# Kernel tuning notes

Hardware: AMD Instinct MI355X
Metric: run time of the kernel (lower is better)

## Reference

```python
import jax, jax.numpy as jnp
import numpy as np

HIDDEN = 1024


def setup_inputs() -> dict:
    key = jax.random.key(0)
    ks = jax.random.split(key, 8)
    B, S, H = 64, 2048, HIDDEN
    scale = 1.0 / np.sqrt(H)
    return {
        "decoder_hidden": jax.random.normal(ks[0], (B, H), jnp.float32),
        "encoder_outputs": jax.random.normal(ks[1], (B, S, 2 * H), jnp.float32),
        "coverage": jax.random.uniform(ks[2], (B, S), jnp.float32),
        "mask": jnp.ones((B, S), jnp.int32),
        # parameters (nn.Linear weight layout: (out, in); we store transposed for x @ W)
        "W_h": jax.random.normal(ks[3], (2 * H, H), jnp.float32) * scale,
        "W_d": jax.random.normal(ks[4], (H, H), jnp.float32) * scale,
        "W_c": jax.random.normal(ks[5], (1, H), jnp.float32) * scale,
        "v": jax.random.normal(ks[6], (H, 1), jnp.float32) * scale,
    }


def reference(decoder_hidden, encoder_outputs, coverage, mask, W_h, W_d, W_c, v):
    # energy: (B, S, H) = tanh(enc@W_h + dec@W_d broadcast over S + coverage*W_c)
    enc_proj = jnp.einsum("bse,eh->bsh", encoder_outputs, W_h)
    dec_proj = (decoder_hidden @ W_d)[:, None, :]            # (B,1,H)
    cov_proj = coverage[:, :, None] * W_c[0][None, None, :]  # (B,S,H)
    energy = jnp.tanh(enc_proj + dec_proj + cov_proj)
    scores = jnp.einsum("bsh,h->bs", energy, v[:, 0])        # (B,S)
    scores = jnp.where(mask == 0, jnp.float32(-10000.0), scores)
    attn_weights = jax.nn.softmax(scores, axis=1)            # (B,S)
    coverage_new = coverage + attn_weights
    context = jnp.einsum("bs,bse->be", attn_weights, encoder_outputs)  # (B,2H)
    return (context, attn_weights, coverage_new)
```

## Files before the change

### kernel.cpp

```cpp
#include <hip/hip_runtime.h>
#include <hip/hip_bf16.h>
#include <stdint.h>

#define BATCH 64
#define SEQ   2048
#define HID   1024
#define EDIM  2048

#define BM 64
#define BN 512
#define BK 32
#define KSTEPS (EDIM / BK)
#define BS (BATCH * SEQ)
#define SMEM_BYTES 76032

typedef __bf16 bf16x8 __attribute__((ext_vector_type(8)));
typedef float  f32x4a __attribute__((ext_vector_type(4)));

__device__ __forceinline__ unsigned short f2bf(float x) {
    __hip_bfloat16 h = __float2bfloat16(x);
    return __builtin_bit_cast(unsigned short, h);
}

__device__ __forceinline__ uint4 pack8(f32x4a f0, f32x4a f1) {
    uint4 r;
    r.x = (unsigned)f2bf(f0.x) | ((unsigned)f2bf(f0.y) << 16);
    r.y = (unsigned)f2bf(f0.z) | ((unsigned)f2bf(f0.w) << 16);
    r.z = (unsigned)f2bf(f1.x) | ((unsigned)f2bf(f1.y) << 16);
    r.w = (unsigned)f2bf(f1.z) | ((unsigned)f2bf(f1.w) << 16);
    return r;
}

__device__ __forceinline__ void gload16(const void* g, void* l) {
    __builtin_amdgcn_global_load_lds(
        (const __attribute__((address_space(1))) void*)g,
        (__attribute__((address_space(3))) void*)l, 16, 0, 0);
}

__device__ __forceinline__ f32x4a ntload4(const float* p) {
    return __builtin_nontemporal_load((const f32x4a*)p);
}

__device__ __forceinline__ int a_addr(int row, int g) {
    int slot = g ^ ((row & 3) ^ ((row >> 2) & 3));
    return (row << 6) + (slot << 4);
}

__global__ void wh_transpose_kernel(const float* __restrict__ Wh,
                                    unsigned short* __restrict__ Wt) {
    __shared__ float tile[32][33];
    int bx = blockIdx.x & 63;
    int by = blockIdx.x >> 6;
    int e0 = bx * 32, h0 = by * 32;
    int tx = threadIdx.x & 31, ty = threadIdx.x >> 5;
    #pragma unroll
    for (int i = 0; i < 4; ++i)
        tile[ty + 8 * i][tx] = Wh[(size_t)(e0 + ty + 8 * i) * HID + h0 + tx];
    __syncthreads();
    if (ty < 4) {
        uint4 wv;
        unsigned short* ws = (unsigned short*)&wv;
        #pragma unroll
        for (int j = 0; j < 8; ++j) ws[j] = f2bf(tile[ty * 8 + j][tx]);
        *(uint4*)&Wt[(size_t)((e0 >> 3) + ty) * 8192 + (size_t)(h0 + tx) * 8] = wv;
    }
}

__global__ void dec_proj_kernel(const float* __restrict__ dec,
                                const float* __restrict__ Wd,
                                float* __restrict__ dp) {
    int gid = blockIdx.x * 256 + threadIdx.x;
    int b = gid >> 10, h = gid & 1023;
    const float* dr = dec + b * HID;
    float acc = 0.f;
    #pragma unroll 4
    for (int k = 0; k < HID; ++k) acc = fmaf(dr[k], Wd[(size_t)k * HID + h], acc);
    dp[gid] = acc;
}

#define MFMA16(a, bfv, c) __builtin_amdgcn_mfma_f32_16x16x32_bf16(a, bfv, c, 0, 0, 0)

__global__ __launch_bounds__(512, 4) void scores_kernel(
    const float* __restrict__ enc, const float* __restrict__ cov,
    const unsigned short* __restrict__ Wt, const float* __restrict__ dp,
    const float* __restrict__ Wc, const float* __restrict__ vv,
    float* __restrict__ spart_out)
{
    extern __shared__ char smem[];
    unsigned short* BlS = (unsigned short*)smem;
    char*  AlB   = smem + 65536;
    float* cov_s = (float*)(smem + 73728);
    float* sred  = (float*)(smem + 73984);

    const int tid  = threadIdx.x;
    const int lane = tid & 63;
    const int wid  = tid >> 6;
    const int wm   = wid >> 2;
    const int wn   = wid & 3;
    const int c15  = lane & 15;
    const int g4   = lane >> 4;

    const int bid  = blockIdx.x;
    const int half = bid & 1;
    const int m    = bid >> 1;
    const int b    = m >> 5;
    const int s0   = (m & 31) * BM;

    const float* Abase = enc + (size_t)(b * SEQ + s0) * EDIM;
    const int arow = tid >> 2;
    const int ag   = tid & 3;

    const unsigned short* Bsrc = Wt + half * 4096 + (size_t)tid * 8;

    f32x4a acc[2][8];
    #pragma unroll
    for (int mi = 0; mi < 2; ++mi)
        #pragma unroll
        for (int nj = 0; nj < 8; ++nj)
            #pragma unroll
            for (int r = 0; r < 4; ++r) acc[mi][nj][r] = 0.f;

    if (tid < BM) cov_s[tid] = cov[b * SEQ + s0 + tid];

    {
        #pragma unroll
        for (int j = 0; j < 4; ++j)
            gload16(Bsrc + (size_t)j * 8192, BlS + j * 4096 + tid * 8);
        if (tid < 256) {
            const float* ap = Abase + (size_t)arow * EDIM + ag * 8;
            *(uint4*)(AlB + a_addr(arow, ag)) = pack8(ntload4(ap), ntload4(ap + 4));
        }
    }
    __syncthreads();

    for (int kk = 0; kk < KSTEPS; ++kk) {
        const int cur = kk & 1, nxt = cur ^ 1;
        const unsigned short* Bcur = BlS + cur * 16384;
        const char* Acur = AlB + cur * 4096;
        f32x4a a0n, a1n;

        if (kk + 1 < KSTEPS) {
            const unsigned short* bs = Bsrc + (size_t)(kk + 1) * 32768;
            unsigned short* bd = BlS + nxt * 16384 + tid * 8;
            #pragma unroll
            for (int j = 0; j < 4; ++j)
                gload16(bs + (size_t)j * 8192, bd + j * 4096);
            if (tid < 256) {
                const float* ap = Abase + (size_t)arow * EDIM + (kk + 1) * BK + ag * 8;
                a0n = ntload4(ap); a1n = ntload4(ap + 4);
            }
        }

        bf16x8 afr0 = *(const bf16x8*)(Acur + a_addr(wm * 32 + c15, g4));
        bf16x8 afr1 = *(const bf16x8*)(Acur + a_addr(wm * 32 + 16 + c15, g4));
        #pragma unroll
        for (int nj = 0; nj < 8; ++nj) {
            bf16x8 bfr = *(const bf16x8*)(Bcur + (size_t)g4 * 4096 +
                                          (size_t)(wn * 128 + nj * 16 + c15) * 8);
            acc[0][nj] = MFMA16(afr0, bfr, acc[0][nj]);
            acc[1][nj] = MFMA16(afr1, bfr, acc[1][nj]);
        }

        if (kk + 1 < KSTEPS && tid < 256)
            *(uint4*)(AlB + nxt * 4096 + a_addr(arow, ag)) = pack8(a0n, a1n);
        __syncthreads();
    }

    float spart[2][4] = {{0.f,0.f,0.f,0.f},{0.f,0.f,0.f,0.f}};
    #pragma unroll
    for (int nj = 0; nj < 8; ++nj) {
        const int h = half * BN + wn * 128 + nj * 16 + c15;
        const float dv  = dp[b * HID + h];
        const float wcv = Wc[h];
        const float vvv = vv[h];
        #pragma unroll
        for (int mi = 0; mi < 2; ++mi) {
            #pragma unroll
            for (int r = 0; r < 4; ++r) {
                const int row = wm * 32 + mi * 16 + g4 * 4 + r;
                float pre = acc[mi][nj][r] + dv + cov_s[row] * wcv;
                float pc = fminf(pre, 20.0f);
                float e2 = __expf(2.0f * pc);
                spart[mi][r] = fmaf((e2 - 1.0f) / (e2 + 1.0f), vvv, spart[mi][r]);
            }
        }
    }
    #pragma unroll
    for (int mi = 0; mi < 2; ++mi) {
        #pragma unroll
        for (int r = 0; r < 4; ++r) {
            float x = spart[mi][r];
            x += __shfl_xor(x, 1);
            x += __shfl_xor(x, 2);
            x += __shfl_xor(x, 4);
            x += __shfl_xor(x, 8);
            if (c15 == 0) sred[(wm * 32 + mi * 16 + g4 * 4 + r) * 4 + wn] = x;
        }
    }
    __syncthreads();
    if (tid < BM) {
        float s = sred[tid * 4] + sred[tid * 4 + 1] + sred[tid * 4 + 2] + sred[tid * 4 + 3];
        spart_out[(size_t)half * BS + b * SEQ + s0 + tid] = s;
    }
}

__global__ void softmax_kernel(const float* __restrict__ spart,
                               const int* __restrict__ mask,
                               const float* __restrict__ cov,
                               float* __restrict__ out)
{
    __shared__ float red[8];
    int b = blockIdx.x, tid = threadIdx.x;
    float vals[8];
    float mx = -1e30f;
    #pragma unroll
    for (int i = 0; i < 8; ++i) {
        int s = tid + i * 256;
        float sc = spart[b * SEQ + s] + spart[BS + b * SEQ + s];
        sc = (mask[b * SEQ + s] == 0) ? -10000.0f : sc;
        vals[i] = sc;
        mx = fmaxf(mx, sc);
    }
    for (int m = 1; m < 64; m <<= 1) mx = fmaxf(mx, __shfl_xor(mx, m));
    if ((tid & 63) == 0) red[tid >> 6] = mx;
    __syncthreads();
    mx = fmaxf(fmaxf(red[0], red[1]), fmaxf(red[2], red[3]));
    float sum = 0.f;
    #pragma unroll
    for (int i = 0; i < 8; ++i) { vals[i] = __expf(vals[i] - mx); sum += vals[i]; }
    for (int m = 1; m < 64; m <<= 1) sum += __shfl_xor(sum, m);
    if ((tid & 63) == 0) red[4 + (tid >> 6)] = sum;
    __syncthreads();
    sum = red[4] + red[5] + red[6] + red[7];
    float inv = 1.0f / sum;
    float* attn = out + BATCH * EDIM;
    float* covn = attn + BATCH * SEQ;
    #pragma unroll
    for (int i = 0; i < 8; ++i) {
        int s = tid + i * 256;
        float w = vals[i] * inv;
        attn[b * SEQ + s] = w;
        covn[b * SEQ + s] = cov[b * SEQ + s] + w;
    }
}

__global__ void context_partial_kernel(const float* __restrict__ enc,
                                       const float* __restrict__ attn,
                                       float* __restrict__ cpart)
{
    __shared__ float w_s[512];
    int bid = blockIdx.x;
    int sc = bid & 3;
    int e0 = ((bid >> 2) & 7) * 256;
    int b  = bid >> 5;
    int tid = threadIdx.x;
    w_s[tid] = attn[b * SEQ + sc * 512 + tid];
    w_s[tid + 256] = attn[b * SEQ + sc * 512 + 256 + tid];
    __syncthreads();
    const float* ep = enc + ((size_t)b * SEQ + sc * 512) * EDIM + e0 + tid;
    float acc = 0.f;
    #pragma unroll 8
    for (int s = 0; s < 512; ++s)
        acc = fmaf(w_s[s], __builtin_nontemporal_load(ep + (size_t)s * EDIM), acc);
    cpart[((size_t)sc * BATCH + b) * EDIM + e0 + tid] = acc;
}

__global__ void ctx_reduce_kernel(const float* __restrict__ cpart,
                                  float* __restrict__ ctx)
{
    int idx = blockIdx.x * 256 + threadIdx.x;
    ctx[idx] = cpart[idx] + cpart[BATCH * EDIM + idx] +
               cpart[2 * BATCH * EDIM + idx] + cpart[3 * BATCH * EDIM + idx];
}

extern "C" void kernel_launch(void* const* d_in, const int* in_sizes, int n_in,
                              void* d_out, int out_size, void* d_ws, size_t ws_size,
                              hipStream_t stream) {
    const float* dec  = (const float*)d_in[0];
    const float* enc  = (const float*)d_in[1];
    const float* cov  = (const float*)d_in[2];
    const int*   mask = (const int*)d_in[3];
    const float* Wh   = (const float*)d_in[4];
    const float* Wd   = (const float*)d_in[5];
    const float* Wc   = (const float*)d_in[6];
    const float* v    = (const float*)d_in[7];
    float* out = (float*)d_out;

    unsigned short* Wt = (unsigned short*)d_ws;
    float* dp    = (float*)((char*)d_ws + (size_t)HID * EDIM * 2);
    float* spart = dp + BATCH * HID;
    float* cpart = spart + 2 * BS;

    (void)hipFuncSetAttribute((const void*)scores_kernel,
                              hipFuncAttributeMaxDynamicSharedMemorySize, SMEM_BYTES);

    wh_transpose_kernel<<<dim3(64 * 32), dim3(256), 0, stream>>>(Wh, Wt);
    dec_proj_kernel<<<dim3(BATCH * HID / 256), dim3(256), 0, stream>>>(dec, Wd, dp);
    scores_kernel<<<dim3((BS / BM) * 2), dim3(512), SMEM_BYTES, stream>>>(
        enc, cov, Wt, dp, Wc, v, spart);
    softmax_kernel<<<dim3(BATCH), dim3(256), 0, stream>>>(spart, mask, cov, out);
    context_partial_kernel<<<dim3(BATCH * 8 * 4), dim3(256), 0, stream>>>(
        enc, out + BATCH * EDIM, cpart);
    ctx_reduce_kernel<<<dim3(BATCH * EDIM / 256), dim3(256), 0, stream>>>(cpart, out);
}
```

Measured before the change: 1.063 ms.

## Load W_h fragments directly from global into registers, drop LDS staging of B

The scores GEMM no longer stages the bf16 W_h tile in shared memory via global_load_lds. Each wave now reads its B fragments straight from global memory (L2-resident) into registers and covers all 64 rows with a 4x4 MFMA tile instead of a 2x8 tile per wave. Shared memory use drops to about 9 KB, which could allow more resident blocks. In exchange, B loads are no longer prefetched and are issued synchronously each k-step, so global latency may be exposed and L2 traffic rises because no B data is shared through LDS.

```diff
diff --git a/kernel.cpp b/kernel.cpp
--- a/kernel.cpp
+++ b/kernel.cpp
@@ -12,7 +12,6 @@
 #define BK 32
 #define KSTEPS (EDIM / BK)
 #define BS (BATCH * SEQ)
-#define SMEM_BYTES 76032
 
 typedef __bf16 bf16x8 __attribute__((ext_vector_type(8)));
 typedef float  f32x4a __attribute__((ext_vector_type(4)));
@@ -29,12 +28,6 @@
     r.z = (unsigned)f2bf(f1.x) | ((unsigned)f2bf(f1.y) << 16);
     r.w = (unsigned)f2bf(f1.z) | ((unsigned)f2bf(f1.w) << 16);
     return r;
-}
-
-__device__ __forceinline__ void gload16(const void* g, void* l) {
-    __builtin_amdgcn_global_load_lds(
-        (const __attribute__((address_space(1))) void*)g,
-        (__attribute__((address_space(3))) void*)l, 16, 0, 0);
 }
 
 __device__ __forceinline__ f32x4a ntload4(const float* p) {
@@ -86,17 +79,13 @@
     const float* __restrict__ Wc, const float* __restrict__ vv,
     float* __restrict__ spart_out)
 {
-    extern __shared__ char smem[];
-    unsigned short* BlS = (unsigned short*)smem;
-    char*  AlB   = smem + 65536;
-    float* cov_s = (float*)(smem + 73728);
-    float* sred  = (float*)(smem + 73984);
+    __shared__ char Al[2][4096];
+    __shared__ float cov_s[BM];
+    __shared__ float sred[BM][8];
 
     const int tid  = threadIdx.x;
     const int lane = tid & 63;
     const int wid  = tid >> 6;
-    const int wm   = wid >> 2;
-    const int wn   = wid & 3;
     const int c15  = lane & 15;
     const int g4   = lane >> 4;
 
@@ -110,74 +99,73 @@
     const int arow = tid >> 2;
     const int ag   = tid & 3;
 
-    const unsigned short* Bsrc = Wt + half * 4096 + (size_t)tid * 8;
-
-    f32x4a acc[2][8];
-    #pragma unroll
-    for (int mi = 0; mi < 2; ++mi)
-        #pragma unroll
-        for (int nj = 0; nj < 8; ++nj)
+    const unsigned short* bptr =
+        Wt + (size_t)g4 * 8192 + (size_t)(half * BN + wid * 64 + c15) * 8;
+
+    f32x4a acc[4][4];
+    #pragma unroll
+    for (int mi = 0; mi < 4; ++mi)
+        #pragma unroll
+        for (int nj = 0; nj < 4; ++nj)
             #pragma unroll
             for (int r = 0; r < 4; ++r) acc[mi][nj][r] = 0.f;
 
     if (tid < BM) cov_s[tid] = cov[b * SEQ + s0 + tid];
 
-    {
-        #pragma unroll
-        for (int j = 0; j < 4; ++j)
-            gload16(Bsrc + (size_t)j * 8192, BlS + j * 4096 + tid * 8);
-        if (tid < 256) {
-            const float* ap = Abase + (size_t)arow * EDIM + ag * 8;
-            *(uint4*)(AlB + a_addr(arow, ag)) = pack8(ntload4(ap), ntload4(ap + 4));
-        }
+    if (tid < 256) {
+        const float* ap = Abase + (size_t)arow * EDIM + ag * 8;
+        *(uint4*)(Al[0] + a_addr(arow, ag)) = pack8(ntload4(ap), ntload4(ap + 4));
     }
     __syncthreads();
 
     for (int kk = 0; kk < KSTEPS; ++kk) {
         const int cur = kk & 1, nxt = cur ^ 1;
-        const unsigned short* Bcur = BlS + cur * 16384;
-        const char* Acur = AlB + cur * 4096;
+
+        bf16x8 bfr[4];
+        #pragma unroll
+        for (int nj = 0; nj < 4; ++nj)
+            bfr[nj] = *(const bf16x8*)(bptr + nj * 128);
+        bptr += 4 * 8192;
+
         f32x4a a0n, a1n;
-
-        if (kk + 1 < KSTEPS) {
-            const unsigned short* bs = Bsrc + (size_t)(kk + 1) * 32768;
-            unsigned short* bd = BlS + nxt * 16384 + tid * 8;
+        if (kk + 1 < KSTEPS && tid < 256) {
+            const float* ap = Abase + (size_t)arow * EDIM + (kk + 1) * BK + ag * 8;
+            a0n = ntload4(ap); a1n = ntload4(ap + 4);
+        }
+
+        bf16x8 afr[4];
+        #pragma unroll
+        for (int mi = 0; mi < 4; ++mi)
+            afr[mi] = *(const bf16x8*)(Al[cur] + a_addr(mi * 16 + c15, g4));
+
+        #pragma unroll
+        for (int mi = 0; mi < 4; ++mi)
             #pragma unroll
-            for (int j = 0; j < 4; ++j)
-                gload16(bs + (size_t)j * 8192, bd + j * 4096);
-            if (tid < 256) {
-                const float* ap = Abase + (size_t)arow * EDIM + (kk + 1) * BK + ag * 8;
-                a0n = ntload4(ap); a1n = ntload4(ap + 4);
-            }
-        }
-
-        bf16x8 afr0 = *(const bf16x8*)(Acur + a_addr(wm * 32 + c15, g4));
-        bf16x8 afr1 = *(const bf16x8*)(Acur + a_addr(wm * 32 + 16 + c15, g4));
-        #pragma unroll
-        for (int nj = 0; nj < 8; ++nj) {
-            bf16x8 bfr = *(const bf16x8*)(Bcur + (size_t)g4 * 4096 +
-                                          (size_t)(wn * 128 + nj * 16 + c15) * 8);
-            acc[0][nj] = MFMA16(afr0, bfr, acc[0][nj]);
-            acc[1][nj] = MFMA16(afr1, bfr, acc[1][nj]);
-        }
+            for (int nj = 0; nj < 4; ++nj)
+                acc[mi][nj] = MFMA16(afr[mi], bfr[nj], acc[mi][nj]);
 
         if (kk + 1 < KSTEPS && tid < 256)
-            *(uint4*)(AlB + nxt * 4096 + a_addr(arow, ag)) = pack8(a0n, a1n);
+            *(uint4*)(Al[nxt] + a_addr(arow, ag)) = pack8(a0n, a1n);
         __syncthreads();
     }
 
-    float spart[2][4] = {{0.f,0.f,0.f,0.f},{0.f,0.f,0.f,0.f}};
-    #pragma unroll
-    for (int nj = 0; nj < 8; ++nj) {
-        const int h = half * BN + wn * 128 + nj * 16 + c15;
+    float spart[4][4];
+    #pragma unroll
+    for (int mi = 0; mi < 4; ++mi)
+        #pragma unroll
+        for (int r = 0; r < 4; ++r) spart[mi][r] = 0.f;
+
+    #pragma unroll
+    for (int nj = 0; nj < 4; ++nj) {
+        const int h = half * BN + wid * 64 + nj * 16 + c15;
         const float dv  = dp[b * HID + h];
         const float wcv = Wc[h];
         const float vvv = vv[h];
         #pragma unroll
-        for (int mi = 0; mi < 2; ++mi) {
+        for (int mi = 0; mi < 4; ++mi) {
             #pragma unroll
             for (int r = 0; r < 4; ++r) {
-                const int row = wm * 32 + mi * 16 + g4 * 4 + r;
+                const int row = mi * 16 + g4 * 4 + r;
                 float pre = acc[mi][nj][r] + dv + cov_s[row] * wcv;
                 float pc = fminf(pre, 20.0f);
                 float e2 = __expf(2.0f * pc);
@@ -186,7 +174,7 @@
         }
     }
     #pragma unroll
-    for (int mi = 0; mi < 2; ++mi) {
+    for (int mi = 0; mi < 4; ++mi) {
         #pragma unroll
         for (int r = 0; r < 4; ++r) {
             float x = spart[mi][r];
@@ -194,12 +182,14 @@
             x += __shfl_xor(x, 2);
             x += __shfl_xor(x, 4);
             x += __shfl_xor(x, 8);
-            if (c15 == 0) sred[(wm * 32 + mi * 16 + g4 * 4 + r) * 4 + wn] = x;
+            if (c15 == 0) sred[mi * 16 + g4 * 4 + r][wid] = x;
         }
     }
     __syncthreads();
     if (tid < BM) {
-        float s = sred[tid * 4] + sred[tid * 4 + 1] + sred[tid * 4 + 2] + sred[tid * 4 + 3];
+        float s = 0.f;
+        #pragma unroll
+        for (int w = 0; w < 8; ++w) s += sred[tid][w];
         spart_out[(size_t)half * BS + b * SEQ + s0 + tid] = s;
     }
 }
@@ -291,12 +281,9 @@
     float* spart = dp + BATCH * HID;
     float* cpart = spart + 2 * BS;
 
-    (void)hipFuncSetAttribute((const void*)scores_kernel,
-                              hipFuncAttributeMaxDynamicSharedMemorySize, SMEM_BYTES);
-
     wh_transpose_kernel<<<dim3(64 * 32), dim3(256), 0, stream>>>(Wh, Wt);
     dec_proj_kernel<<<dim3(BATCH * HID / 256), dim3(256), 0, stream>>>(dec, Wd, dp);
-    scores_kernel<<<dim3((BS / BM) * 2), dim3(512), SMEM_BYTES, stream>>>(
+    scores_kernel<<<dim3((BS / BM) * 2), dim3(512), 0, stream>>>(
         enc, cov, Wt, dp, Wc, v, spart);
     softmax_kernel<<<dim3(BATCH), dim3(256), 0, stream>>>(spart, mask, cov, out);
     context_partial_kernel<<<dim3(BATCH * 8 * 4), dim3(256), 0, stream>>>(
```

After: 1.049 ms. About the same (-1.4%).
